# Optimization experiments

Measured on AMD Instinct MI355X. Metric: run time of the kernel, lower is better.

## Reference

```python
import jax, jax.numpy as jnp
import numpy as np
import math

EMBED_DIM = 1024
N_HEADS = 16
HEAD_DIM = EMBED_DIM // N_HEADS
B, N = 2, 2048


def setup_inputs() -> dict:
    key = jax.random.key(0)
    k1, k2, k3 = jax.random.split(key, 3)
    x = jax.random.normal(k1, (B, N, EMBED_DIM), dtype=jnp.float32)
    # Per-head Linear(D, 3*head_dim), stacked over heads. PyTorch Linear init scale ~1/sqrt(fan_in).
    bound = 1.0 / math.sqrt(EMBED_DIM)
    Wkqv = jax.random.uniform(k2, (N_HEADS, EMBED_DIM, 3 * HEAD_DIM), dtype=jnp.float32, minval=-bound, maxval=bound)
    bkqv = jax.random.uniform(k3, (N_HEADS, 3 * HEAD_DIM), dtype=jnp.float32, minval=-bound, maxval=bound)
    return {"x": x, "Wkqv": Wkqv, "bkqv": bkqv}


def reference(x, Wkqv, bkqv):
    Bx, Nx, D = x.shape
    hd = Wkqv.shape[-1] // 3
    # all heads at once: [B, H, N, 3*hd]
    proj = jnp.einsum('bnd,hdf->bhnf', x, Wkqv) + bkqv[None, :, None, :]
    # torch.split order in the original is (k, q, v)
    k, q, v = jnp.split(proj, 3, axis=-1)
    # scores = q @ k^T / sqrt(head_dim)   [B, H, N, N]
    scores = jnp.einsum('bhqd,bhkd->bhqk', q, k) / math.sqrt(hd)
    causal = jnp.tril(jnp.ones((Nx, Nx), dtype=bool))
    scores = jnp.where(causal[None, None, :, :], scores, -jnp.inf)
    attn = jax.nn.softmax(scores, axis=-1)
    out = jnp.einsum('bhqk,bhkd->bhqd', attn, v)  # [B, H, N, hd]
    # concat heads -> [B, N, D]  (forward() passes no out_matrix, so no output projection)
    return out.transpose(0, 2, 1, 3).reshape(Bx, Nx, D)
```

## Files before the change

### kernel.cpp

```cpp
#include <hip/hip_runtime.h>
#include <math.h>

typedef float f32x4 __attribute__((ext_vector_type(4)));
typedef __bf16 bf16x8 __attribute__((ext_vector_type(8)));

#define MFMA16(a, b, c) __builtin_amdgcn_mfma_f32_16x16x32_bf16((a), (b), (c), 0, 0, 0)

constexpr int Bsz = 2, Nseq = 2048, Dm = 1024, Hh = 16, HDim = 64, F3 = 192;
constexpr int Mrows = Bsz * Nseq;
constexpr int NC = Hh * F3;
constexpr float QSCALE = 0.125f * 1.4426950408889634f;

__device__ inline void load_lds16(const void* g, void* l) {
    __builtin_amdgcn_global_load_lds((const __attribute__((address_space(1))) void*)g,
                                     (__attribute__((address_space(3))) void*)l, 16, 0, 0);
}

#define FENCE asm volatile("" ::: "memory")
#define BARRIER do { FENCE; __builtin_amdgcn_s_barrier(); FENCE; } while (0)

__global__ __launch_bounds__(256) void conv_x_kernel(const float* __restrict__ x,
                                                     __bf16* __restrict__ xb) {
    int i = blockIdx.x * 256 + threadIdx.x;
    const float4* xv = reinterpret_cast<const float4*>(x);
    float4 a = xv[2 * i];
    float4 b = xv[2 * i + 1];
    bf16x8 o = {(__bf16)a.x, (__bf16)a.y, (__bf16)a.z, (__bf16)a.w,
                (__bf16)b.x, (__bf16)b.y, (__bf16)b.z, (__bf16)b.w};
    *reinterpret_cast<bf16x8*>(xb + 8 * i) = o;
}

__global__ __launch_bounds__(256) void conv_w_kernel(const float* __restrict__ w,
                                                     __bf16* __restrict__ wt) {
    __shared__ __bf16 tile[32][66];
    int h = blockIdx.z, d0 = blockIdx.x * 32, c0 = blockIdx.y * 64;
    for (int i = threadIdx.x; i < 32 * 64; i += 256) {
        int di = i >> 6, cj = i & 63;
        tile[di][cj] = (__bf16)w[(size_t)(h * Dm + d0 + di) * F3 + c0 + cj];
    }
    __syncthreads();
    for (int i = threadIdx.x; i < 32 * 64; i += 256) {
        int ci = i >> 5, dj = i & 31;
        wt[(size_t)(h * F3 + c0 + ci) * Dm + d0 + dj] = tile[dj][ci];
    }
}

__global__ __launch_bounds__(512, 2) void gemm_proj(const __bf16* __restrict__ xb,
                                                    const __bf16* __restrict__ wt,
                                                    const float* __restrict__ bias,
                                                    __bf16* __restrict__ kbuf,
                                                    __bf16* __restrict__ qbuf,
                                                    __bf16* __restrict__ vt) {
    __shared__ __align__(16) __bf16 Ab[2][256 * 64];
    __shared__ __align__(16) __bf16 Bb[2][192 * 64];

    int flat = blockIdx.x;
    int swz = (flat & 7) * 32 + (flat >> 3);
    int bm = swz >> 4, bn = swz & 15;
    int r0 = bm * 256, n0 = bn * 192;

    int w = threadIdx.x >> 6, lane = threadIdx.x & 63;
    int col = lane & 15, quad = lane >> 4;
    int wm = w >> 2, wn = w & 3;

    f32x4 acc[8][3] = {};

    int rl = lane >> 3;
    int cg = ((lane & 7) ^ rl) * 8;

    auto stage = [&](int t, int s) {
#pragma unroll
        for (int i = 0; i < 4; i++) {
            int rowb = w * 32 + i * 8;
            load_lds16(xb + (size_t)(r0 + rowb + rl) * Dm + t * 64 + cg,
                       &Ab[s][rowb * 64]);
        }
#pragma unroll
        for (int i = 0; i < 3; i++) {
            int rowb = w * 24 + i * 8;
            load_lds16(wt + (size_t)(n0 + rowb + rl) * Dm + t * 64 + cg,
                       &Bb[s][rowb * 64]);
        }
    };

    stage(0, 0);
    stage(1, 1);

    for (int j = 0; j < 16; j++) {
        int s = j & 1;
        if (j < 15) asm volatile("s_waitcnt vmcnt(7)" ::: "memory");
        else        asm volatile("s_waitcnt vmcnt(0)" ::: "memory");
        BARRIER;

#pragma unroll
        for (int ks = 0; ks < 2; ks++) {
            int cq = ks * 4 + quad;
            bf16x8 af[8], bfr[3];
#pragma unroll
            for (int mt = 0; mt < 8; mt++) {
                int row = wm * 128 + mt * 16 + col;
                af[mt] = *reinterpret_cast<const bf16x8*>(
                    &Ab[s][row * 64 + ((cq ^ (row & 7)) * 8)]);
            }
#pragma unroll
            for (int nt = 0; nt < 3; nt++) {
                int row = wn * 48 + nt * 16 + col;
                bfr[nt] = *reinterpret_cast<const bf16x8*>(
                    &Bb[s][row * 64 + ((cq ^ (row & 7)) * 8)]);
            }
            __builtin_amdgcn_s_setprio(1);
#pragma unroll
            for (int mt = 0; mt < 8; mt++)
#pragma unroll
                for (int nt = 0; nt < 3; nt++)
                    acc[mt][nt] = MFMA16(af[mt], bfr[nt], acc[mt][nt]);
            __builtin_amdgcn_s_setprio(0);
        }

        BARRIER;
        if (j + 2 < 16) stage(j + 2, s);
    }

#pragma unroll
    for (int nt = 0; nt < 3; nt++) {
        int g = n0 + wn * 48 + nt * 16 + col;
        int h = g / F3, c = g - h * F3;
        float bv = bias[g];
        bool isq = (c >= 64 && c < 128), isv = (c >= 128);
        int cd = c & 63;
#pragma unroll
        for (int mt = 0; mt < 8; mt++) {
#pragma unroll
            for (int rg = 0; rg < 4; rg++) {
                int r = r0 + wm * 128 + mt * 16 + quad * 4 + rg;
                int b = r >> 11, n = r & (Nseq - 1);
                float v = acc[mt][nt][rg] + bv;
                if (isq) v *= QSCALE;
                size_t bh = (size_t)(b * Hh + h);
                if (isv) vt[(bh * HDim + cd) * Nseq + n] = (__bf16)v;
                else ((isq) ? qbuf : kbuf)[(bh * Nseq + n) * HDim + cd] = (__bf16)v;
            }
        }
    }
}

__global__ __launch_bounds__(256) void proj_small(const float* __restrict__ x,
                                                  const __bf16* __restrict__ wt,
                                                  const float* __restrict__ bias,
                                                  __bf16* __restrict__ kbuf,
                                                  __bf16* __restrict__ qbuf,
                                                  __bf16* __restrict__ vt) {
    int h = blockIdx.y;
    int wave = threadIdx.x >> 6, lane = threadIdx.x & 63;
    int col = lane & 15, quad = lane >> 4;
    int r0 = blockIdx.x * 128 + wave * 32;

    f32x4 acc[12][2] = {};
    const float* xr0 = x + (size_t)(r0 + col) * Dm + quad * 8;
    const float* xr1 = xr0 + 16 * Dm;
    const __bf16* wbase = wt + (size_t)(h * F3 + col) * Dm + quad * 8;

    for (int k0 = 0; k0 < Dm; k0 += 32) {
        float4 a0lo = *reinterpret_cast<const float4*>(xr0 + k0);
        float4 a0hi = *reinterpret_cast<const float4*>(xr0 + k0 + 4);
        float4 a1lo = *reinterpret_cast<const float4*>(xr1 + k0);
        float4 a1hi = *reinterpret_cast<const float4*>(xr1 + k0 + 4);
        bf16x8 a0 = {(__bf16)a0lo.x, (__bf16)a0lo.y, (__bf16)a0lo.z, (__bf16)a0lo.w,
                     (__bf16)a0hi.x, (__bf16)a0hi.y, (__bf16)a0hi.z, (__bf16)a0hi.w};
        bf16x8 a1 = {(__bf16)a1lo.x, (__bf16)a1lo.y, (__bf16)a1lo.z, (__bf16)a1lo.w,
                     (__bf16)a1hi.x, (__bf16)a1hi.y, (__bf16)a1hi.z, (__bf16)a1hi.w};
#pragma unroll
        for (int ct = 0; ct < 12; ct++) {
            bf16x8 bf = *reinterpret_cast<const bf16x8*>(wbase + ct * 16 * Dm + k0);
            acc[ct][0] = MFMA16(a0, bf, acc[ct][0]);
            acc[ct][1] = MFMA16(a1, bf, acc[ct][1]);
        }
    }
#pragma unroll
    for (int ct = 0; ct < 12; ct++) {
        int c = ct * 16 + col;
        float bv = bias[h * F3 + c];
        int cd = c & 63;
        bool isq = (c >= 64 && c < 128), isv = (c >= 128);
#pragma unroll
        for (int rt = 0; rt < 2; rt++) {
#pragma unroll
            for (int rg = 0; rg < 4; rg++) {
                int r = r0 + rt * 16 + quad * 4 + rg;
                int b = r >> 11, n = r & (Nseq - 1);
                float v = acc[ct][rt][rg] + bv;
                if (isq) v *= QSCALE;
                size_t bh = (size_t)(b * Hh + h);
                if (isv) vt[(bh * HDim + cd) * Nseq + n] = (__bf16)v;
                else ((isq) ? qbuf : kbuf)[(bh * Nseq + n) * HDim + cd] = (__bf16)v;
            }
        }
    }
}

__global__ __launch_bounds__(256) void attn_kernel(const __bf16* __restrict__ qbuf,
                                                   const __bf16* __restrict__ kbuf,
                                                   const __bf16* __restrict__ vt,
                                                   float* __restrict__ out) {
    __shared__ __align__(16) __bf16 Kb[2][64 * 64];
    __shared__ __align__(16) __bf16 Vb[2][64 * 64];
    __shared__ __align__(16) __bf16 plds[4][16][72];
    int bh = blockIdx.x;
    int b = bh >> 4, h = bh & 15;
    int tile = 31 - blockIdx.y;
    int wave = threadIdx.x >> 6, lane = threadIdx.x & 63;
    int col = lane & 15, quad = lane >> 4;
    int q0 = tile * 64 + wave * 16;

    const __bf16* qbase = qbuf + (size_t)bh * Nseq * HDim;
    const __bf16* kbase = kbuf + (size_t)bh * Nseq * HDim;
    const __bf16* vbase = vt + (size_t)bh * HDim * Nseq;

    bf16x8 aq0 = *reinterpret_cast<const bf16x8*>(qbase + (q0 + col) * HDim + quad * 8);
    bf16x8 aq1 = *reinterpret_cast<const bf16x8*>(qbase + (q0 + col) * HDim + quad * 8 + 32);

    f32x4 o[4] = {};
    float lsum[4] = {0.f, 0.f, 0.f, 0.f};

    int mb = tile * 64;
    int loop_end = mb + 64;

    int rl = lane >> 3;
    int srow0 = wave * 16 + rl;
    int srow1 = wave * 16 + 8 + rl;
    int sc = (lane & 7) ^ rl;
    const __bf16* ksrc0 = kbase + srow0 * HDim + sc * 8;
    const __bf16* ksrc1 = kbase + srow1 * HDim + sc * 8;
    const __bf16* vsrc0 = vbase + (size_t)srow0 * Nseq + sc * 8;
    const __bf16* vsrc1 = vbase + (size_t)srow1 * Nseq + sc * 8;
    int d0 = wave * 1024, d1 = wave * 1024 + 512;

    int sw0 = ((quad ^ (col & 7)) * 8);
    int sw1 = (((quad + 4) ^ (col & 7)) * 8);

    load_lds16(ksrc0, &Kb[0][d0]);
    load_lds16(ksrc1, &Kb[0][d1]);
    load_lds16(vsrc0, &Vb[0][d0]);
    load_lds16(vsrc1, &Vb[0][d1]);
    FENCE;

    int s = 0;
    for (int kb = 0; kb < loop_end; kb += 64) {
        asm volatile("s_waitcnt vmcnt(0)" ::: "memory");
        BARRIER;
        int nkb = kb + 64;
        if (nkb < loop_end) {
            load_lds16(ksrc0 + nkb * HDim, &Kb[s ^ 1][d0]);
            load_lds16(ksrc1 + nkb * HDim, &Kb[s ^ 1][d1]);
            load_lds16(vsrc0 + nkb, &Vb[s ^ 1][d0]);
            load_lds16(vsrc1 + nkb, &Vb[s ^ 1][d1]);
        }

        bool masked = (kb == mb);
        const __bf16* Kcur = Kb[s];
        const __bf16* Vcur = Vb[s];
        f32x4 z = {};
        f32x4 sc4[4];
#pragma unroll
        for (int g = 0; g < 4; g++) {
            const __bf16* krow = Kcur + (col + 16 * g) * 64;
            bf16x8 k0 = *reinterpret_cast<const bf16x8*>(krow + sw0);
            bf16x8 k1 = *reinterpret_cast<const bf16x8*>(krow + sw1);
            sc4[g] = MFMA16(aq0, k0, z);
            sc4[g] = MFMA16(aq1, k1, sc4[g]);
        }
        if (masked) {
#pragma unroll
            for (int g = 0; g < 4; g++) {
#pragma unroll
                for (int r = 0; r < 4; r++) {
                    int qi = q0 + quad * 4 + r;
                    float p = (kb + col + 16 * g <= qi) ? exp2f(sc4[g][r]) : 0.f;
                    lsum[r] += p;
                    plds[wave][quad * 4 + r][col + 16 * g] = (__bf16)p;
                }
            }
        } else {
#pragma unroll
            for (int g = 0; g < 4; g++) {
#pragma unroll
                for (int r = 0; r < 4; r++) {
                    float p = exp2f(sc4[g][r]);
                    lsum[r] += p;
                    plds[wave][quad * 4 + r][col + 16 * g] = (__bf16)p;
                }
            }
        }
        bf16x8 pa0 = *reinterpret_cast<const bf16x8*>(&plds[wave][col][quad * 8]);
        bf16x8 pa1 = *reinterpret_cast<const bf16x8*>(&plds[wave][col][32 + quad * 8]);
#pragma unroll
        for (int nt = 0; nt < 4; nt++) {
            const __bf16* vrow = Vcur + (col + 16 * nt) * 64;
            bf16x8 v0 = *reinterpret_cast<const bf16x8*>(vrow + sw0);
            bf16x8 v1 = *reinterpret_cast<const bf16x8*>(vrow + sw1);
            o[nt] = MFMA16(pa0, v0, o[nt]);
            o[nt] = MFMA16(pa1, v1, o[nt]);
        }
        s ^= 1;
    }

    float linv[4];
#pragma unroll
    for (int r = 0; r < 4; r++) {
        float t = lsum[r];
        t += __shfl_xor(t, 1);
        t += __shfl_xor(t, 2);
        t += __shfl_xor(t, 4);
        t += __shfl_xor(t, 8);
        linv[r] = 1.f / t;
    }
#pragma unroll
    for (int nt = 0; nt < 4; nt++) {
#pragma unroll
        for (int r = 0; r < 4; r++) {
            int qi = q0 + quad * 4 + r;
            out[((size_t)(b * Nseq + qi)) * Dm + h * HDim + nt * 16 + col] = o[nt][r] * linv[r];
        }
    }
}

extern "C" void kernel_launch(void* const* d_in, const int* in_sizes, int n_in,
                              void* d_out, int out_size, void* d_ws, size_t ws_size,
                              hipStream_t stream) {
    const float* x = nullptr;
    const float* w = nullptr;
    const float* bias = nullptr;
    for (int i = 0; i < n_in; i++) {
        if (in_sizes[i] == Mrows * Dm) x = (const float*)d_in[i];
        else if (in_sizes[i] == Hh * Dm * F3) w = (const float*)d_in[i];
        else if (in_sizes[i] == Hh * F3) bias = (const float*)d_in[i];
    }
    float* outp = (float*)d_out;

    char* ws = (char*)d_ws;
    __bf16* wt = (__bf16*)(ws);
    __bf16* kbuf = (__bf16*)(ws + 6291456);
    __bf16* qbuf = (__bf16*)(ws + 6291456 + 8388608);
    __bf16* vt = (__bf16*)(ws + 6291456 + 2 * 8388608);
    __bf16* xb = (__bf16*)(ws + 6291456 + 3 * 8388608);

    conv_w_kernel<<<dim3(Dm / 32, F3 / 64, Hh), 256, 0, stream>>>(w, wt);
    if (ws_size >= (size_t)(6291456 + 4 * 8388608)) {
        conv_x_kernel<<<Mrows * Dm / (8 * 256), 256, 0, stream>>>(x, xb);
        gemm_proj<<<dim3((Mrows / 256) * (NC / 192)), 512, 0, stream>>>(xb, wt, bias, kbuf, qbuf, vt);
    } else {
        proj_small<<<dim3(Mrows / 128, Hh), 256, 0, stream>>>(x, wt, bias, kbuf, qbuf, vt);
    }
    attn_kernel<<<dim3(32, 32), 256, 0, stream>>>(qbuf, kbuf, vt, outp);
}
```

Baseline: 159.1 us.

## Permute P/V key layout for packed LDS stores and compute row sums via MFMA

```diff
diff --git a/kernel.cpp b/kernel.cpp
--- a/kernel.cpp
+++ b/kernel.cpp
@@ -3,6 +3,7 @@
 
 typedef float f32x4 __attribute__((ext_vector_type(4)));
 typedef __bf16 bf16x8 __attribute__((ext_vector_type(8)));
+typedef __bf16 bf16x4 __attribute__((ext_vector_type(4)));
 
 #define MFMA16(a, b, c) __builtin_amdgcn_mfma_f32_16x16x32_bf16((a), (b), (c), 0, 0, 0)
 
@@ -18,6 +19,7 @@
 
 #define FENCE asm volatile("" ::: "memory")
 #define BARRIER do { FENCE; __builtin_amdgcn_s_barrier(); FENCE; } while (0)
+
 
 __global__ __launch_bounds__(256) void conv_x_kernel(const float* __restrict__ x,
                                                      __bf16* __restrict__ xb) {
@@ -137,8 +139,12 @@
                 float v = acc[mt][nt][rg] + bv;
                 if (isq) v *= QSCALE;
                 size_t bh = (size_t)(b * Hh + h);
-                if (isv) vt[(bh * HDim + cd) * Nseq + n] = (__bf16)v;
-                else ((isq) ? qbuf : kbuf)[(bh * Nseq + n) * HDim + cd] = (__bf16)v;
+                if (isv) {
+                    int np = (n & ~63) | ((n & 15) << 2) | ((n >> 4) & 3);
+                    vt[(bh * HDim + cd) * Nseq + np] = (__bf16)v;
+                } else {
+                    ((isq) ? qbuf : kbuf)[(bh * Nseq + n) * HDim + cd] = (__bf16)v;
+                }
             }
         }
     }
@@ -191,8 +197,12 @@
                 float v = acc[ct][rt][rg] + bv;
                 if (isq) v *= QSCALE;
                 size_t bh = (size_t)(b * Hh + h);
-                if (isv) vt[(bh * HDim + cd) * Nseq + n] = (__bf16)v;
-                else ((isq) ? qbuf : kbuf)[(bh * Nseq + n) * HDim + cd] = (__bf16)v;
+                if (isv) {
+                    int np = (n & ~63) | ((n & 15) << 2) | ((n >> 4) & 3);
+                    vt[(bh * HDim + cd) * Nseq + np] = (__bf16)v;
+                } else {
+                    ((isq) ? qbuf : kbuf)[(bh * Nseq + n) * HDim + cd] = (__bf16)v;
+                }
             }
         }
     }
@@ -219,8 +229,11 @@
     bf16x8 aq0 = *reinterpret_cast<const bf16x8*>(qbase + (q0 + col) * HDim + quad * 8);
     bf16x8 aq1 = *reinterpret_cast<const bf16x8*>(qbase + (q0 + col) * HDim + quad * 8 + 32);
 
+    const bf16x8 vone = {(__bf16)1.f, (__bf16)1.f, (__bf16)1.f, (__bf16)1.f,
+                         (__bf16)1.f, (__bf16)1.f, (__bf16)1.f, (__bf16)1.f};
+
     f32x4 o[4] = {};
-    float lsum[4] = {0.f, 0.f, 0.f, 0.f};
+    f32x4 ls = {};
 
     int mb = tile * 64;
     int loop_end = mb + 64;
@@ -271,28 +284,29 @@
         }
         if (masked) {
 #pragma unroll
-            for (int g = 0; g < 4; g++) {
-#pragma unroll
-                for (int r = 0; r < 4; r++) {
-                    int qi = q0 + quad * 4 + r;
+            for (int r = 0; r < 4; r++) {
+                int qi = q0 + quad * 4 + r;
+                bf16x4 pk;
+#pragma unroll
+                for (int g = 0; g < 4; g++) {
                     float p = (kb + col + 16 * g <= qi) ? exp2f(sc4[g][r]) : 0.f;
-                    lsum[r] += p;
-                    plds[wave][quad * 4 + r][col + 16 * g] = (__bf16)p;
+                    pk[g] = (__bf16)p;
                 }
+                *reinterpret_cast<bf16x4*>(&plds[wave][quad * 4 + r][col * 4]) = pk;
             }
         } else {
 #pragma unroll
-            for (int g = 0; g < 4; g++) {
-#pragma unroll
-                for (int r = 0; r < 4; r++) {
-                    float p = exp2f(sc4[g][r]);
-                    lsum[r] += p;
-                    plds[wave][quad * 4 + r][col + 16 * g] = (__bf16)p;
-                }
+            for (int r = 0; r < 4; r++) {
+                bf16x4 pk;
+#pragma unroll
+                for (int g = 0; g < 4; g++) pk[g] = (__bf16)exp2f(sc4[g][r]);
+                *reinterpret_cast<bf16x4*>(&plds[wave][quad * 4 + r][col * 4]) = pk;
             }
         }
         bf16x8 pa0 = *reinterpret_cast<const bf16x8*>(&plds[wave][col][quad * 8]);
         bf16x8 pa1 = *reinterpret_cast<const bf16x8*>(&plds[wave][col][32 + quad * 8]);
+        ls = MFMA16(pa0, vone, ls);
+        ls = MFMA16(pa1, vone, ls);
 #pragma unroll
         for (int nt = 0; nt < 4; nt++) {
             const __bf16* vrow = Vcur + (col + 16 * nt) * 64;
@@ -306,14 +320,7 @@
 
     float linv[4];
 #pragma unroll
-    for (int r = 0; r < 4; r++) {
-        float t = lsum[r];
-        t += __shfl_xor(t, 1);
-        t += __shfl_xor(t, 2);
-        t += __shfl_xor(t, 4);
-        t += __shfl_xor(t, 8);
-        linv[r] = 1.f / t;
-    }
+    for (int r = 0; r < 4; r++) linv[r] = 1.f / ls[r];
 #pragma unroll
     for (int nt = 0; nt < 4; nt++) {
 #pragma unroll
```

New measurement: 159.2 us. Within noise of the previous version (+0.1%).
